# Optimization experiments

Hardware: AMD Instinct MI355X
Metric: run time of the kernel (lower is better)

Reference implementation:

```python
import jax, jax.numpy as jnp
import numpy as np

N_NODES = 50000
N_EDGES = 500000
IN_CH = 128
OUT_CH = 256


def setup_inputs() -> dict:
    key = jax.random.key(0)
    k1, k2, k3, k4, k5 = jax.random.split(key, 5)
    x = jax.random.normal(k1, (N_NODES, IN_CH), dtype=jnp.float32)
    edge_index = jax.random.randint(k2, (2, N_EDGES), 0, N_NODES, dtype=jnp.int64)
    edge_weight = jax.random.normal(k3, (N_EDGES,), dtype=jnp.float32)
    # GCNConv linear weight (xavier-uniform) and bias (zeros in torch init; use randn for generality)
    limit = float(np.sqrt(6.0 / (IN_CH + OUT_CH)))
    W = jax.random.uniform(k4, (IN_CH, OUT_CH), minval=-limit, maxval=limit, dtype=jnp.float32)
    b = jnp.zeros((OUT_CH,), dtype=jnp.float32)
    return {"x": x, "W": W, "b": b, "edge_index": edge_index, "edge_weight": edge_weight}


def reference(x, W, b, edge_index, edge_weight):
    N = x.shape[0]
    # GCN wrapper applies sigmoid to edge weights before GCNConv
    ew = jax.nn.sigmoid(edge_weight)
    # gcn_norm: add self-loops with weight 1
    loop = jnp.arange(N, dtype=edge_index.dtype)
    row = jnp.concatenate([edge_index[0], loop])  # source nodes
    col = jnp.concatenate([edge_index[1], loop])  # target nodes
    w = jnp.concatenate([ew, jnp.ones((N,), dtype=x.dtype)])
    # degree on target index, symmetric normalization
    deg = jax.ops.segment_sum(w, col, num_segments=N)
    dinv = jnp.where(deg > 0, jax.lax.rsqrt(deg), jnp.zeros_like(deg))
    norm = dinv[row] * w * dinv[col]  # [E+N]
    # linear transform first (GCNConv: lin has no bias; bias added after aggregation)
    h = x @ W  # [N, OUT_CH]
    msg = h[row] * norm[:, None]  # gather + scale  [E+N, OUT_CH]
    out = jax.ops.segment_sum(msg, col, num_segments=N) + b
    return out
```

## Files before the change

### kernel.cpp

```cpp
#include <hip/hip_runtime.h>
#include <hip/hip_bf16.h>
#include <math.h>

#define NN 50000
#define NE 500000
#define IC 128
#define OC 256
#define NPAD 50176
#define NB 196
#define NEB4 489
#define CONVSTRIDE (NEB4 * 256)

typedef short bf16x8 __attribute__((ext_vector_type(8)));
typedef float f32x4 __attribute__((ext_vector_type(4)));

static __device__ inline unsigned short f2b(float f) {
    __hip_bfloat16 h = __float2bfloat16(f);
    return *reinterpret_cast<unsigned short*>(&h);
}
static __device__ inline float b2f(short u) {
    unsigned v = ((unsigned)(unsigned short)u) << 16;
    return __int_as_float(v);
}

__global__ void k_init(unsigned long long* __restrict__ deg64) {
    int i = blockIdx.x * 256 + threadIdx.x;
    deg64[i] = (unsigned long long)(1u << 24);
}

__global__ __launch_bounds__(256) void k_pass1(const int* __restrict__ col,
                        const float* __restrict__ ew,
                        unsigned long long* __restrict__ deg64,
                        int* __restrict__ eord,
                        const float* __restrict__ x,
                        unsigned short* __restrict__ xb,
                        const float* __restrict__ W,
                        unsigned short* __restrict__ WT) {
    const int base = blockIdx.x * 1024 + threadIdx.x;
    int   cs[4];
    float ws[4];
    #pragma unroll
    for (int j = 0; j < 4; ++j) {
        int e = base + j * 256;
        if (e < NE) { cs[j] = col[e]; ws[j] = ew[e]; }
    }
    unsigned long long olds[4];
    #pragma unroll
    for (int j = 0; j < 4; ++j) {
        int e = base + j * 256;
        if (e < NE) {
            float w = 1.0f / (1.0f + expf(-ws[j]));
            unsigned long long pack = (1ull << 32) | (unsigned long long)(unsigned)(w * 16777216.0f);
            olds[j] = atomicAdd(&deg64[cs[j]], pack);
        }
    }
    #pragma unroll
    for (int j = 0; j < 4; ++j) {
        int e = base + j * 256;
        if (e < NE) eord[e] = (int)(olds[j] >> 32);
    }
    const int g = blockIdx.x * 256 + threadIdx.x;
    const int NX = NN * (IC / 4);
    for (int i = g; i < NX; i += CONVSTRIDE) {
        float4 v = ((const float4*)x)[i];
        ushort4 o;
        o.x = f2b(v.x); o.y = f2b(v.y); o.z = f2b(v.z); o.w = f2b(v.w);
        ((ushort4*)xb)[i] = o;
    }
    if (g < IC * OC) {
        int k = g >> 8;
        int n = g & 255;
        WT[n * IC + k] = f2b(W[g]);
    }
}

__global__ void k_dinv_scan(const unsigned long long* __restrict__ deg64,
                            float* __restrict__ dinv,
                            int* __restrict__ sp,
                            int* __restrict__ bsum) {
    __shared__ int s[256];
    int t = threadIdx.x;
    int i = blockIdx.x * 256 + t;
    unsigned long long v = deg64[i];
    int cnt = (int)(v >> 32);
    float deg = (float)(unsigned)v * (1.0f / 16777216.0f);
    dinv[i] = rsqrtf(deg);
    s[t] = cnt;
    __syncthreads();
    #pragma unroll
    for (int off = 1; off < 256; off <<= 1) {
        int add = (t >= off) ? s[t - off] : 0;
        __syncthreads();
        s[t] += add;
        __syncthreads();
    }
    sp[i] = s[t] - cnt;
    if (t == 255) bsum[blockIdx.x] = s[255];
}

__global__ void k_scan2(int* __restrict__ bsum) {
    __shared__ int s[256];
    int t = threadIdx.x;
    int v = (t < NB) ? bsum[t] : 0;
    s[t] = v;
    __syncthreads();
    #pragma unroll
    for (int off = 1; off < 256; off <<= 1) {
        int add = (t >= off) ? s[t - off] : 0;
        __syncthreads();
        s[t] += add;
        __syncthreads();
    }
    if (t < NB) bsum[t] = s[t] - v;
}

__global__ __launch_bounds__(256) void k_fill(const int* __restrict__ row,
                       const int* __restrict__ col,
                       const float* __restrict__ ew,
                       const float* __restrict__ dinv,
                       const int* __restrict__ sp,
                       const int* __restrict__ bsum,
                       const int* __restrict__ eord,
                       int2* __restrict__ epack) {
    const int base = blockIdx.x * 1024 + threadIdx.x;
    #pragma unroll
    for (int j = 0; j < 4; ++j) {
        int e = base + j * 256;
        if (e < NE) {
            int r = row[e], t = col[e];
            float w = 1.0f / (1.0f + expf(-ew[e]));
            float nrm = dinv[r] * w * dinv[t];
            int pos = sp[t] + bsum[t >> 8] + eord[e];
            int2 p;
            p.x = r;
            p.y = __float_as_int(nrm);
            epack[pos] = p;
        }
    }
}

__global__ __launch_bounds__(256) void k_gather(const unsigned short* __restrict__ xb,
                                                const int* __restrict__ sp,
                                                const int* __restrict__ bsum,
                                                const int2* __restrict__ epack,
                                                const float* __restrict__ dinv,
                                                unsigned short* __restrict__ aggb) {
    int n = blockIdx.x * 16 + (threadIdx.x >> 4);
    if (n >= NN) return;
    int lane = threadIdx.x & 15;
    const bf16x8* xv = (const bf16x8*)xb;

    float di = dinv[n];
    float s2 = di * di;
    bf16x8 xs = xv[(size_t)n * 16 + lane];
    float acc[8];
    #pragma unroll
    for (int c = 0; c < 8; ++c) acc[c] = b2f(xs[c]) * s2;

    int s = sp[n] + bsum[n >> 8];
    int t = sp[n + 1] + bsum[(n + 1) >> 8];
    int e = s;
    for (; e + 4 <= t; e += 4) {
        int2 p0 = epack[e];
        int2 p1 = epack[e + 1];
        int2 p2 = epack[e + 2];
        int2 p3 = epack[e + 3];
        bf16x8 v0 = xv[(size_t)p0.x * 16 + lane];
        bf16x8 v1 = xv[(size_t)p1.x * 16 + lane];
        bf16x8 v2 = xv[(size_t)p2.x * 16 + lane];
        bf16x8 v3 = xv[(size_t)p3.x * 16 + lane];
        float w0 = __int_as_float(p0.y);
        float w1 = __int_as_float(p1.y);
        float w2 = __int_as_float(p2.y);
        float w3 = __int_as_float(p3.y);
        #pragma unroll
        for (int c = 0; c < 8; ++c) acc[c] += b2f(v0[c]) * w0;
        #pragma unroll
        for (int c = 0; c < 8; ++c) acc[c] += b2f(v1[c]) * w1;
        #pragma unroll
        for (int c = 0; c < 8; ++c) acc[c] += b2f(v2[c]) * w2;
        #pragma unroll
        for (int c = 0; c < 8; ++c) acc[c] += b2f(v3[c]) * w3;
    }
    for (; e < t; ++e) {
        int2 p = epack[e];
        bf16x8 v = xv[(size_t)p.x * 16 + lane];
        float w = __int_as_float(p.y);
        #pragma unroll
        for (int c = 0; c < 8; ++c) acc[c] += b2f(v[c]) * w;
    }

    bf16x8 o;
    #pragma unroll
    for (int c = 0; c < 8; ++c) o[c] = (short)f2b(acc[c]);
    ((bf16x8*)aggb)[(size_t)n * 16 + lane] = o;
}

__global__ __launch_bounds__(256) void k_gemm(const unsigned short* __restrict__ agg,
                                              const unsigned short* __restrict__ WT,
                                              const float* __restrict__ bias,
                                              float* __restrict__ out) {
    const int w = threadIdx.x >> 6;
    const int lane = threadIdx.x & 63;
    const int m0 = blockIdx.y * 64 + (w >> 1) * 32;
    const int n0 = blockIdx.x * 128 + (w & 1) * 64;
    const int lm = lane & 15;
    const int lk = (lane >> 4) * 8;

    f32x4 acc[2][4] = {};
    #pragma unroll
    for (int ks = 0; ks < 4; ++ks) {
        const int k0 = ks * 32 + lk;
        bf16x8 wf[4], af[2];
        #pragma unroll
        for (int j = 0; j < 4; ++j)
            wf[j] = *(const bf16x8*)(WT + (size_t)(n0 + j * 16 + lm) * IC + k0);
        #pragma unroll
        for (int i = 0; i < 2; ++i)
            af[i] = *(const bf16x8*)(agg + (size_t)(m0 + i * 16 + lm) * IC + k0);
        #pragma unroll
        for (int i = 0; i < 2; ++i)
            #pragma unroll
            for (int j = 0; j < 4; ++j)
                acc[i][j] = __builtin_amdgcn_mfma_f32_16x16x32_bf16(wf[j], af[i], acc[i][j], 0, 0, 0);
    }

    const int mcol = lane & 15;
    const int nb4 = (lane >> 4) * 4;
    #pragma unroll
    for (int i = 0; i < 2; ++i) {
        int m = m0 + i * 16 + mcol;
        if (m < NN) {
            #pragma unroll
            for (int j = 0; j < 4; ++j) {
                int nn = n0 + j * 16 + nb4;
                float4 bv = *(const float4*)&bias[nn];
                float4 o;
                o.x = acc[i][j][0] + bv.x;
                o.y = acc[i][j][1] + bv.y;
                o.z = acc[i][j][2] + bv.z;
                o.w = acc[i][j][3] + bv.w;
                *(float4*)(out + (size_t)m * OC + nn) = o;
            }
        }
    }
}

extern "C" void kernel_launch(void* const* d_in, const int* in_sizes, int n_in,
                              void* d_out, int out_size, void* d_ws, size_t ws_size,
                              hipStream_t stream) {
    const float* x  = (const float*)d_in[0];
    const float* W  = (const float*)d_in[1];
    const float* b  = (const float*)d_in[2];
    const int*   ei = (const int*)d_in[3];
    const float* ew = (const float*)d_in[4];
    const int* row = ei;
    const int* col = ei + NE;
    float* out = (float*)d_out;

    char* w0 = (char*)d_ws;
    unsigned long long* deg64 = (unsigned long long*)w0;  w0 += NPAD * 8;
    float* dinv  = (float*)w0;                   w0 += NPAD * 4;
    int*   sp    = (int*)w0;                     w0 += NPAD * 4;
    int*   bsum  = (int*)w0;                     w0 += 256 * 4;
    int*   eord  = (int*)w0;                     w0 += NE * 4;
    int2*  epack = (int2*)w0;                    w0 += NE * 8;
    unsigned short* WT   = (unsigned short*)w0;  w0 += IC * OC * 2;
    unsigned short* xb   = (unsigned short*)w0;  w0 += (size_t)NN * IC * 2;
    unsigned short* aggb = (unsigned short*)w0;

    k_init      <<<NB, 256, 0, stream>>>(deg64);
    k_pass1     <<<NEB4, 256, 0, stream>>>(col, ew, deg64, eord, x, xb, W, WT);
    k_dinv_scan <<<NB, 256, 0, stream>>>(deg64, dinv, sp, bsum);
    k_scan2     <<<1, 256, 0, stream>>>(bsum);
    k_fill      <<<NEB4, 256, 0, stream>>>(row, col, ew, dinv, sp, bsum, eord, epack);
    k_gather    <<<(NN + 15) / 16, 256, 0, stream>>>(xb, sp, bsum, epack, dinv, aggb);
    k_gemm      <<<dim3(2, (NN + 63) / 64), 256, 0, stream>>>(aggb, WT, b, out);
}
```

Measured before the change: 178.0 us.

## Sort nodes by in-degree for load-balanced gather and retile GEMM to 16-row blocks

Builds a degree histogram and a counting-sort permutation of nodes by in-degree, then has the gather kernel process nodes in that order. Nodes with similar edge counts share a wavefront, which is meant to cut divergence from uneven degrees. The GEMM is also retiled so each block covers 16 rows by all 256 output columns, launched as 3125 blocks. This adds a histogram pass, a permutation kernel and an extra indirection. The gather's scattered writes may hurt locality.

```diff
diff --git a/kernel.cpp b/kernel.cpp
--- a/kernel.cpp
+++ b/kernel.cpp
@@ -23,9 +23,10 @@
     return __int_as_float(v);
 }
 
-__global__ void k_init(unsigned long long* __restrict__ deg64) {
+__global__ void k_init(unsigned long long* __restrict__ deg64, int* __restrict__ dhist) {
     int i = blockIdx.x * 256 + threadIdx.x;
     deg64[i] = (unsigned long long)(1u << 24);
+    if (blockIdx.x == 0) dhist[threadIdx.x] = 0;
 }
 
 __global__ __launch_bounds__(256) void k_pass1(const int* __restrict__ col,
@@ -77,9 +78,12 @@
 __global__ void k_dinv_scan(const unsigned long long* __restrict__ deg64,
                             float* __restrict__ dinv,
                             int* __restrict__ sp,
-                            int* __restrict__ bsum) {
+                            int* __restrict__ bsum,
+                            int* __restrict__ dhist) {
     __shared__ int s[256];
+    __shared__ int h[256];
     int t = threadIdx.x;
+    h[t] = 0;
     int i = blockIdx.x * 256 + t;
     unsigned long long v = deg64[i];
     int cnt = (int)(v >> 32);
@@ -96,9 +100,14 @@
     }
     sp[i] = s[t] - cnt;
     if (t == 255) bsum[blockIdx.x] = s[255];
-}
-
-__global__ void k_scan2(int* __restrict__ bsum) {
+    if (i < NN) atomicAdd(&h[min(cnt, 255)], 1);
+    __syncthreads();
+    if (h[t]) atomicAdd(&dhist[t], h[t]);
+}
+
+__global__ void k_scan2(int* __restrict__ bsum,
+                        const int* __restrict__ dhist,
+                        int* __restrict__ dcursor) {
     __shared__ int s[256];
     int t = threadIdx.x;
     int v = (t < NB) ? bsum[t] : 0;
@@ -112,6 +121,39 @@
         __syncthreads();
     }
     if (t < NB) bsum[t] = s[t] - v;
+    __syncthreads();
+    int v2 = dhist[t];
+    s[t] = v2;
+    __syncthreads();
+    #pragma unroll
+    for (int off = 1; off < 256; off <<= 1) {
+        int add = (t >= off) ? s[t - off] : 0;
+        __syncthreads();
+        s[t] += add;
+        __syncthreads();
+    }
+    dcursor[t] = s[t] - v2;
+}
+
+__global__ void k_perm(const unsigned long long* __restrict__ deg64,
+                       int* __restrict__ dcursor,
+                       int* __restrict__ perm) {
+    __shared__ int h[256];
+    __shared__ int base[256];
+    int t = threadIdx.x;
+    h[t] = 0;
+    __syncthreads();
+    int i = blockIdx.x * 256 + t;
+    int bin = -1, local = 0;
+    if (i < NN) {
+        int cnt = (int)(deg64[i] >> 32);
+        bin = min(cnt, 255);
+        local = atomicAdd(&h[bin], 1);
+    }
+    __syncthreads();
+    if (h[t]) base[t] = atomicAdd(&dcursor[t], h[t]);
+    __syncthreads();
+    if (i < NN) perm[base[bin] + local] = i;
 }
 
 __global__ __launch_bounds__(256) void k_fill(const int* __restrict__ row,
@@ -144,9 +186,11 @@
                                                 const int* __restrict__ bsum,
                                                 const int2* __restrict__ epack,
                                                 const float* __restrict__ dinv,
+                                                const int* __restrict__ perm,
                                                 unsigned short* __restrict__ aggb) {
-    int n = blockIdx.x * 16 + (threadIdx.x >> 4);
-    if (n >= NN) return;
+    int idx = blockIdx.x * 16 + (threadIdx.x >> 4);
+    if (idx >= NN) return;
+    int n = perm[idx];
     int lane = threadIdx.x & 15;
     const bf16x8* xv = (const bf16x8*)xb;
 
@@ -202,47 +246,38 @@
                                               float* __restrict__ out) {
     const int w = threadIdx.x >> 6;
     const int lane = threadIdx.x & 63;
-    const int m0 = blockIdx.y * 64 + (w >> 1) * 32;
-    const int n0 = blockIdx.x * 128 + (w & 1) * 64;
+    const int m0 = blockIdx.x * 16;
+    const int n0 = w * 64;
     const int lm = lane & 15;
     const int lk = (lane >> 4) * 8;
 
-    f32x4 acc[2][4] = {};
+    f32x4 acc[4] = {};
     #pragma unroll
     for (int ks = 0; ks < 4; ++ks) {
         const int k0 = ks * 32 + lk;
-        bf16x8 wf[4], af[2];
+        bf16x8 af = *(const bf16x8*)(agg + (size_t)(m0 + lm) * IC + k0);
+        bf16x8 wf[4];
         #pragma unroll
         for (int j = 0; j < 4; ++j)
             wf[j] = *(const bf16x8*)(WT + (size_t)(n0 + j * 16 + lm) * IC + k0);
         #pragma unroll
-        for (int i = 0; i < 2; ++i)
-            af[i] = *(const bf16x8*)(agg + (size_t)(m0 + i * 16 + lm) * IC + k0);
-        #pragma unroll
-        for (int i = 0; i < 2; ++i)
-            #pragma unroll
-            for (int j = 0; j < 4; ++j)
-                acc[i][j] = __builtin_amdgcn_mfma_f32_16x16x32_bf16(wf[j], af[i], acc[i][j], 0, 0, 0);
+        for (int j = 0; j < 4; ++j)
+            acc[j] = __builtin_amdgcn_mfma_f32_16x16x32_bf16(wf[j], af, acc[j], 0, 0, 0);
     }
 
     const int mcol = lane & 15;
     const int nb4 = (lane >> 4) * 4;
-    #pragma unroll
-    for (int i = 0; i < 2; ++i) {
-        int m = m0 + i * 16 + mcol;
-        if (m < NN) {
-            #pragma unroll
-            for (int j = 0; j < 4; ++j) {
-                int nn = n0 + j * 16 + nb4;
-                float4 bv = *(const float4*)&bias[nn];
-                float4 o;
-                o.x = acc[i][j][0] + bv.x;
-                o.y = acc[i][j][1] + bv.y;
-                o.z = acc[i][j][2] + bv.z;
-                o.w = acc[i][j][3] + bv.w;
-                *(float4*)(out + (size_t)m * OC + nn) = o;
-            }
-        }
+    const int m = m0 + mcol;
+    #pragma unroll
+    for (int j = 0; j < 4; ++j) {
+        int nn = n0 + j * 16 + nb4;
+        float4 bv = *(const float4*)&bias[nn];
+        float4 o;
+        o.x = acc[j][0] + bv.x;
+        o.y = acc[j][1] + bv.y;
+        o.z = acc[j][2] + bv.z;
+        o.w = acc[j][3] + bv.w;
+        *(float4*)(out + (size_t)m * OC + nn) = o;
     }
 }
 
@@ -263,17 +298,21 @@
     float* dinv  = (float*)w0;                   w0 += NPAD * 4;
     int*   sp    = (int*)w0;                     w0 += NPAD * 4;
     int*   bsum  = (int*)w0;                     w0 += 256 * 4;
+    int*   dhist = (int*)w0;                     w0 += 256 * 4;
+    int*   dcursor = (int*)w0;                   w0 += 256 * 4;
+    int*   perm  = (int*)w0;                     w0 += NPAD * 4;
     int*   eord  = (int*)w0;                     w0 += NE * 4;
     int2*  epack = (int2*)w0;                    w0 += NE * 8;
     unsigned short* WT   = (unsigned short*)w0;  w0 += IC * OC * 2;
     unsigned short* xb   = (unsigned short*)w0;  w0 += (size_t)NN * IC * 2;
     unsigned short* aggb = (unsigned short*)w0;
 
-    k_init      <<<NB, 256, 0, stream>>>(deg64);
+    k_init      <<<NB, 256, 0, stream>>>(deg64, dhist);
     k_pass1     <<<NEB4, 256, 0, stream>>>(col, ew, deg64, eord, x, xb, W, WT);
-    k_dinv_scan <<<NB, 256, 0, stream>>>(deg64, dinv, sp, bsum);
-    k_scan2     <<<1, 256, 0, stream>>>(bsum);
+    k_dinv_scan <<<NB, 256, 0, stream>>>(deg64, dinv, sp, bsum, dhist);
+    k_scan2     <<<1, 256, 0, stream>>>(bsum, dhist, dcursor);
+    k_perm      <<<NB, 256, 0, stream>>>(deg64, dcursor, perm);
     k_fill      <<<NEB4, 256, 0, stream>>>(row, col, ew, dinv, sp, bsum, eord, epack);
-    k_gather    <<<(NN + 15) / 16, 256, 0, stream>>>(xb, sp, bsum, epack, dinv, aggb);
-    k_gemm      <<<dim3(2, (NN + 63) / 64), 256, 0, stream>>>(aggb, WT, b, out);
-}
+    k_gather    <<<(NN + 15) / 16, 256, 0, stream>>>(xb, sp, bsum, epack, dinv, perm, aggb);
+    k_gemm      <<<3125, 256, 0, stream>>>(aggb, WT, b, out);
+}
```

Result: slower. 198.2 us (+11.3%).
